# Kernel tuning notes

Hardware: AMD Instinct MI355X
Metric: run time of the kernel (lower is better)

Reference implementation:

```python
import jax, jax.numpy as jnp
import numpy as np

B, C, Himg, Wimg = 32, 256, 64, 64
P = 8            # partition (window) size
HEADS, DH = 8, 32
SEQ = P * P      # tokens per window = 64
SCALE = C ** (-0.5)  # note: feat_dim**-0.5, as in the source
EPS = 1e-5


def _relative_position_index(h, w):
    coords = np.stack(np.meshgrid(np.arange(h), np.arange(w), indexing='ij'))  # [2,h,w]
    cf = coords.reshape(2, -1)
    rel = cf[:, :, None] - cf[:, None, :]            # [2,hw,hw]
    rel = rel.transpose(1, 2, 0)
    rel[:, :, 0] += h - 1
    rel[:, :, 1] += w - 1
    rel[:, :, 0] *= 2 * w - 1
    return rel.sum(-1)                               # [hw,hw] int

REL_IDX = jnp.asarray(_relative_position_index(P, P).reshape(-1))  # [SEQ*SEQ]


def layernorm(x, g, b):
    mu = jnp.mean(x, -1, keepdims=True)
    var = jnp.mean(jnp.square(x - mu), -1, keepdims=True)
    return (x - mu) * jax.lax.rsqrt(var + EPS) * g + b


def setup_inputs() -> dict:
    key = jax.random.key(0)
    ks = jax.random.split(key, 12)
    d = {}
    d['x'] = jax.random.normal(ks[0], (B, C, Himg, Wimg), jnp.float32)
    d['ln1_g'] = jnp.ones((C,), jnp.float32)
    d['ln1_b'] = jnp.zeros((C,), jnp.float32)
    d['qkv_w'] = jax.random.normal(ks[1], (C, 3 * C), jnp.float32) * 0.02
    d['qkv_b'] = jnp.zeros((3 * C,), jnp.float32)
    d['merge_w'] = jax.random.normal(ks[2], (C, C), jnp.float32) * 0.02
    d['merge_b'] = jnp.zeros((C,), jnp.float32)
    d['bias_table'] = jax.random.normal(ks[3], ((2 * P - 1) * (2 * P - 1), HEADS), jnp.float32) * 0.02
    d['ln2_g'] = jnp.ones((C,), jnp.float32)
    d['ln2_b'] = jnp.zeros((C,), jnp.float32)
    d['mlp_w1'] = jax.random.normal(ks[4], (C, 4 * C), jnp.float32) * 0.02
    d['mlp_b1'] = jnp.zeros((4 * C,), jnp.float32)
    d['mlp_w2'] = jax.random.normal(ks[5], (4 * C, C), jnp.float32) * 0.02
    d['mlp_b2'] = jnp.zeros((C,), jnp.float32)
    return d


def reference(x, ln1_g, ln1_b, qkv_w, qkv_b, merge_w, merge_b, bias_table,
              ln2_g, ln2_b, mlp_w1, mlp_b1, mlp_w2, mlp_b2):
    Bn, Cn, H, W = x.shape
    hp, wp = H // P, W // P
    # window partition: [B,C,H,W] -> [B, G, P*P, C]
    xw = x.reshape(Bn, Cn, hp, P, wp, P).transpose(0, 2, 4, 3, 5, 1)
    xw = xw.reshape(Bn, hp * wp, P * P, Cn)

    # --- attention block ---
    h = layernorm(xw, ln1_g, ln1_b)
    qkv = h @ qkv_w + qkv_b                                    # [B,G,S,3C]
    q, k, v = jnp.split(qkv, 3, axis=-1)
    def heads(t):
        return t.reshape(Bn, hp * wp, SEQ, HEADS, DH).transpose(0, 1, 3, 2, 4)
    q, k, v = heads(q), heads(k) * SCALE, heads(v)             # [B,G,h,S,d]
    scores = jnp.einsum('bghid,bghjd->bghij', q, k)            # [B,G,h,S,S]
    rel_bias = bias_table[REL_IDX].reshape(SEQ, SEQ, HEADS).transpose(2, 0, 1)
    attn = jax.nn.softmax(scores + rel_bias[None, None], axis=-1)
    out = jnp.einsum('bghij,bghjd->bghid', attn, v)            # [B,G,h,S,d]
    out = out.transpose(0, 1, 3, 2, 4).reshape(Bn, hp * wp, SEQ, Cn)
    xw = xw + (out @ merge_w + merge_b)

    # --- MLP block ---
    h = layernorm(xw, ln2_g, ln2_b)
    h = jax.nn.gelu(h @ mlp_w1 + mlp_b1, approximate=False)
    xw = xw + (h @ mlp_w2 + mlp_b2)

    # window departition: [B,G,P*P,C] -> [B,C,H,W]
    y = xw.reshape(Bn, hp, wp, P, P, Cn).transpose(0, 5, 1, 3, 2, 4)
    return y.reshape(Bn, Cn, hp * P, wp * P)
```

## Files before the change

kernel.cpp:

```cpp
#include <hip/hip_runtime.h>

typedef __attribute__((ext_vector_type(8))) short short8;
typedef __attribute__((ext_vector_type(8))) unsigned short ushort8v;
typedef __attribute__((ext_vector_type(4))) float f32x4;
typedef __attribute__((ext_vector_type(4))) int int4v;
typedef __attribute__((ext_vector_type(4))) unsigned short ushort4v;
typedef __attribute__((ext_vector_type(2))) unsigned short ushort2v;

#define SCALE_F 0.0625f
#define EPS_F 1e-5f

__device__ __forceinline__ float bf2f(unsigned short u) {
  unsigned int i = ((unsigned int)u) << 16;
  return __builtin_bit_cast(float, i);
}
__device__ __forceinline__ unsigned short f2bf(float f) {
  unsigned int i = __builtin_bit_cast(unsigned int, f);
  i += 0x7fffu + ((i >> 16) & 1u);
  return (unsigned short)(i >> 16);
}

__device__ __forceinline__ void gload_lds16(const unsigned short* g, unsigned short* l) {
  __builtin_amdgcn_global_load_lds(
      (const __attribute__((address_space(1))) void*)g,
      (__attribute__((address_space(3))) void*)l, 16, 0, 0);
}

template<int K, int N>
__global__ void cast_wt(const float* __restrict__ src, unsigned short* __restrict__ dst) {
  int id = blockIdx.x * 256 + threadIdx.x;
  if (id >= K * N) return;
  int k = id % K, n = id / K;
  dst[id] = f2bf(src[(size_t)k * N + n]);
}

__global__ void build_relb(const float* __restrict__ table, float* __restrict__ relb) {
  int id = blockIdx.x * 256 + threadIdx.x;
  int h = id >> 12, i = (id >> 6) & 63, j = id & 63;
  int dy = (i >> 3) - (j >> 3) + 7;
  int dx = (i & 7) - (j & 7) + 7;
  relb[id] = table[(dy * 15 + dx) * 8 + h];
}

#define PLN_RS 264
__global__ __launch_bounds__(256) void part_ln1(
    const float* __restrict__ x, const float* __restrict__ g, const float* __restrict__ bb,
    unsigned short* __restrict__ h) {
  __shared__ __align__(16) unsigned short t_lds[128 * PLN_RS];
  __shared__ float ps_sum[128][2];
  __shared__ float ps_ss[128][2];
  const int tid = threadIdx.x;
  const int bid = blockIdx.x;
  const int b = bid >> 5, wr = (bid >> 2) & 7, cp = bid & 3;
  const int r0 = wr * 8;
  const int c0 = cp * 16;

  const int q = tid & 3, r = (tid >> 2) & 7, cb = tid >> 5;
  const float* xb = x + (size_t)b * 256 * 4096 + (size_t)(r0 + r) * 64 + c0 + q * 4;
#pragma unroll
  for (int it = 0; it < 16; it++) {
    int cpair = it * 8 + cb;
    const float* p0 = xb + (size_t)(2 * cpair) * 4096;
    f32x4 v0 = *(const f32x4*)p0;
    f32x4 v1 = *(const f32x4*)(p0 + 4096);
#pragma unroll
    for (int j = 0; j < 4; j++) {
      int px = r * 16 + q * 4 + j;
      ushort2v u = { f2bf(v0[j]), f2bf(v1[j]) };
      *(ushort2v*)(&t_lds[px * PLN_RS + 2 * cpair]) = u;
    }
  }
  __syncthreads();

  {
    const int p = tid & 127, half = tid >> 7;
    float sum = 0.f, ss = 0.f;
#pragma unroll
    for (int i = 0; i < 16; i++) {
      ushort8v u = *(const ushort8v*)(&t_lds[p * PLN_RS + half * 128 + i * 8]);
#pragma unroll
      for (int e = 0; e < 8; e++) { float f = bf2f(u[e]); sum += f; ss += f * f; }
    }
    ps_sum[p][half] = sum;
    ps_ss[p][half] = ss;
  }
  __syncthreads();

#pragma unroll
  for (int w = 0; w < 16; w++) {
    int id = w * 256 + tid;
    int p = id >> 5, ch = id & 31;
    float mu = (ps_sum[p][0] + ps_sum[p][1]) * (1.f / 256.f);
    float var = (ps_ss[p][0] + ps_ss[p][1]) * (1.f / 256.f) - mu * mu;
    float rs = rsqrtf(var + EPS_F);
    ushort8v u = *(const ushort8v*)(&t_lds[p * PLN_RS + ch * 8]);
    f32x4 g0 = *(const f32x4*)(g + ch * 8);
    f32x4 g1 = *(const f32x4*)(g + ch * 8 + 4);
    f32x4 b0 = *(const f32x4*)(bb + ch * 8);
    f32x4 b1 = *(const f32x4*)(bb + ch * 8 + 4);
    ushort8v o;
#pragma unroll
    for (int e = 0; e < 4; e++) {
      o[e]     = f2bf((bf2f(u[e])     - mu) * rs * g0[e] + b0[e]);
      o[e + 4] = f2bf((bf2f(u[e + 4]) - mu) * rs * g1[e] + b1[e]);
    }
    int rr = p >> 4, col = p & 15;
    size_t m = (size_t)b * 4096 + (size_t)(wr * 8 + cp * 2 + (col >> 3)) * 64 + rr * 8 + (col & 7);
    *(ushort8v*)(h + m * 256 + ch * 8) = o;
  }
}

__global__ __launch_bounds__(256) void ln2k(
    const unsigned short* __restrict__ x2, const float* __restrict__ g, const float* __restrict__ bb,
    unsigned short* __restrict__ h2) {
  int m = blockIdx.x * 4 + (threadIdx.x >> 6);
  int l = threadIdx.x & 63;
  ushort4v u = *(const ushort4v*)(x2 + (size_t)m * 256 + l * 4);
  float v[4];
  float sum = 0.f, ss = 0.f;
#pragma unroll
  for (int j = 0; j < 4; j++) { v[j] = bf2f(u[j]); sum += v[j]; ss += v[j] * v[j]; }
#pragma unroll
  for (int d = 1; d < 64; d <<= 1) {
    sum += __shfl_xor(sum, d, 64);
    ss  += __shfl_xor(ss, d, 64);
  }
  float mu = sum * (1.f / 256.f);
  float var = ss * (1.f / 256.f) - mu * mu;
  float rs = rsqrtf(var + EPS_F);
  ushort4v oh;
#pragma unroll
  for (int j = 0; j < 4; j++) {
    int c = l * 4 + j;
    oh[j] = f2bf((v[j] - mu) * rs * g[c] + bb[c]);
  }
  *(ushort4v*)(h2 + (size_t)m * 256 + l * 4) = oh;
}

enum { EPI_QKV = 0, EPI_MERGE = 1, EPI_GELU = 2, EPI_OUT = 3 };

template<int EPI>
__device__ __forceinline__ void gemm_body(
    unsigned short* As, unsigned short* Bs,
    const unsigned short* __restrict__ A, const unsigned short* __restrict__ Bt,
    const float* __restrict__ bias, const void* __restrict__ res,
    void* __restrict__ out, int K, int N, long m_base) {
  const int tid = threadIdx.x;
  const int l15 = tid & 15, lhi = (tid & 63) >> 4;
  const int wid = tid >> 6, wm = wid >> 1, wn = wid & 1;
  const size_t m0 = (size_t)blockIdx.x * 128;
  const int n0 = blockIdx.y * 128;
  const int row_s = tid >> 3, kc8 = (tid & 7) * 8;

  auto stage = [&](int kb, int k0) {
#pragma unroll
    for (int i = 0; i < 4; i++) {
      int row = i * 32 + row_s;
      gload_lds16(A + (m0 + row) * (size_t)K + k0 + kc8, &As[kb * 8192 + (i * 256 + tid) * 8]);
      gload_lds16(Bt + (size_t)(n0 + row) * (size_t)K + k0 + kc8, &Bs[kb * 8192 + (i * 256 + tid) * 8]);
    }
  };

  f32x4 acc[4][4];
#pragma unroll
  for (int i = 0; i < 4; i++)
#pragma unroll
    for (int j = 0; j < 4; j++) acc[i][j] = (f32x4){0.f, 0.f, 0.f, 0.f};

  stage(0, 0);
  int kb = 0;
  for (int k0 = 0; k0 < K; k0 += 64, kb ^= 1) {
    if (k0 + 64 < K) {
      stage(kb ^ 1, k0 + 64);
      asm volatile("s_waitcnt vmcnt(8)" ::: "memory");
    } else {
      asm volatile("s_waitcnt vmcnt(0)" ::: "memory");
    }
    __builtin_amdgcn_s_barrier();
#pragma unroll
    for (int ks = 0; ks < 2; ks++) {
      short8 af[4], bfr[4];
#pragma unroll
      for (int t = 0; t < 4; t++) {
        af[t]  = *(const short8*)(&As[kb * 8192 + (wm * 64 + t * 16 + l15) * 64 + ks * 32 + lhi * 8]);
        bfr[t] = *(const short8*)(&Bs[kb * 8192 + (wn * 64 + t * 16 + l15) * 64 + ks * 32 + lhi * 8]);
      }
#pragma unroll
      for (int mt = 0; mt < 4; mt++)
#pragma unroll
        for (int nt = 0; nt < 4; nt++)
          acc[mt][nt] = __builtin_amdgcn_mfma_f32_16x16x32_bf16(af[mt], bfr[nt], acc[mt][nt], 0, 0, 0);
    }
    __builtin_amdgcn_s_barrier();
  }

#pragma unroll
  for (int mt = 0; mt < 4; mt++) {
#pragma unroll
    for (int nt = 0; nt < 4; nt++) {
      const size_t gml0 = m0 + wm * 64 + mt * 16 + lhi * 4;
      const size_t gm0 = gml0 + (size_t)m_base;
      const int gn = n0 + wn * 64 + nt * 16 + l15;
      if (EPI == EPI_QKV) {
#pragma unroll
        for (int r = 0; r < 4; r++)
          ((unsigned short*)out)[(gml0 + r) * (size_t)N + gn] = f2bf(acc[mt][nt][r] + bias[gn]);
      } else if (EPI == EPI_MERGE) {
        int bi = (int)(gm0 >> 12), gg = (int)((gm0 >> 6) & 63), s0 = (int)(gm0 & 63);
        size_t sp = (size_t)((gg >> 3) * 8 + (s0 >> 3)) * 64 + (gg & 7) * 8 + (s0 & 7);
        f32x4 xr = *(const f32x4*)(&((const float*)res)[((size_t)(bi * 256 + gn)) * 4096 + sp]);
#pragma unroll
        for (int r = 0; r < 4; r++)
          ((unsigned short*)out)[(gm0 + r) * 256 + gn] = f2bf(acc[mt][nt][r] + bias[gn] + xr[r]);
      } else if (EPI == EPI_GELU) {
#pragma unroll
        for (int r = 0; r < 4; r++) {
          float v = acc[mt][nt][r] + bias[gn];
          float gl = 0.5f * v * (1.f + erff(v * 0.70710678118f));
          ((unsigned short*)out)[(gml0 + r) * (size_t)N + gn] = f2bf(gl);
        }
      } else {
        int bi = (int)(gm0 >> 12), gg = (int)((gm0 >> 6) & 63), s0 = (int)(gm0 & 63);
        size_t sp = (size_t)((gg >> 3) * 8 + (s0 >> 3)) * 64 + (gg & 7) * 8 + (s0 & 7);
        f32x4 o4;
#pragma unroll
        for (int r = 0; r < 4; r++)
          o4[r] = acc[mt][nt][r] + bias[gn] + bf2f(((const unsigned short*)res)[(gm0 + r) * 256 + gn]);
        *(f32x4*)(&((float*)out)[((size_t)(bi * 256 + gn)) * 4096 + sp]) = o4;
      }
    }
  }
}

#define GEMM_WRAP(name, epi)                                                          \
__global__ __launch_bounds__(256) void name(                                          \
    const unsigned short* __restrict__ A, const unsigned short* __restrict__ Bt,      \
    const float* __restrict__ bias, const void* __restrict__ res,                     \
    void* __restrict__ out, int K, int N, long m_base) {                              \
  __shared__ __align__(16) unsigned short As[2 * 128 * 64];                           \
  __shared__ __align__(16) unsigned short Bs[2 * 128 * 64];                           \
  gemm_body<epi>(As, Bs, A, Bt, bias, res, out, K, N, m_base);                        \
}
GEMM_WRAP(gemm_qkv, EPI_QKV)
GEMM_WRAP(gemm_merge, EPI_MERGE)
GEMM_WRAP(gemm_gelu, EPI_GELU)
GEMM_WRAP(gemm_out, EPI_OUT)

__global__ __launch_bounds__(64) void attn_k(
    const unsigned short* __restrict__ qkv, const float* __restrict__ relb,
    unsigned short* __restrict__ o) {
  __shared__ __align__(16) unsigned short p_lds[64 * 72];
  __shared__ __align__(16) unsigned short vt_lds[32 * 72];
  const int l = threadIdx.x;
  const int l15 = l & 15, lhi = l >> 4;
  const int w = blockIdx.x, head = blockIdx.y;
  const unsigned short* base = qkv + (size_t)w * 64 * 768 + head * 32;

  short8 aq[4], bk[4];
#pragma unroll
  for (int t = 0; t < 4; t++) {
    aq[t] = *(const short8*)(base + (t * 16 + l15) * 768 + lhi * 8);
    bk[t] = *(const short8*)(base + 256 + (t * 16 + l15) * 768 + lhi * 8);
  }
  f32x4 s[4][4];
#pragma unroll
  for (int i = 0; i < 4; i++)
#pragma unroll
    for (int j = 0; j < 4; j++) s[i][j] = (f32x4){0.f, 0.f, 0.f, 0.f};
#pragma unroll
  for (int mt = 0; mt < 4; mt++)
#pragma unroll
    for (int nt = 0; nt < 4; nt++)
      s[mt][nt] = __builtin_amdgcn_mfma_f32_16x16x32_bf16(aq[mt], bk[nt], s[mt][nt], 0, 0, 0);

  const float* rb = relb + head * 4096;
  float rsum[4][4];
#pragma unroll
  for (int mt = 0; mt < 4; mt++) {
#pragma unroll
    for (int r = 0; r < 4; r++) {
      int row = mt * 16 + lhi * 4 + r;
      float vv[4];
      float vmax = -1e30f;
#pragma unroll
      for (int nt = 0; nt < 4; nt++) {
        int col = nt * 16 + l15;
        float v = s[mt][nt][r] * SCALE_F + rb[row * 64 + col];
        vv[nt] = v;
        vmax = fmaxf(vmax, v);
      }
#pragma unroll
      for (int d = 1; d < 16; d <<= 1) vmax = fmaxf(vmax, __shfl_xor(vmax, d, 64));
      float sum = 0.f;
#pragma unroll
      for (int nt = 0; nt < 4; nt++) {
        float p = __expf(vv[nt] - vmax);
        sum += p;
        p_lds[row * 72 + nt * 16 + l15] = f2bf(p);
      }
#pragma unroll
      for (int d = 1; d < 16; d <<= 1) sum += __shfl_xor(sum, d, 64);
      rsum[mt][r] = 1.f / sum;
    }
  }

#pragma unroll
  for (int j = 0; j < 4; j++) {
    short8 vv = *(const short8*)(base + 512 + l * 768 + j * 8);
#pragma unroll
    for (int e = 0; e < 8; e++)
      vt_lds[(j * 8 + e) * 72 + l] = (unsigned short)vv[e];
  }
  __syncthreads();

  f32x4 o2[4][2];
#pragma unroll
  for (int i = 0; i < 4; i++) { o2[i][0] = (f32x4){0.f,0.f,0.f,0.f}; o2[i][1] = (f32x4){0.f,0.f,0.f,0.f}; }
#pragma unroll
  for (int ks = 0; ks < 2; ks++) {
    short8 ap[4], bv[2];
#pragma unroll
    for (int t = 0; t < 4; t++)
      ap[t] = *(const short8*)(&p_lds[(t * 16 + l15) * 72 + ks * 32 + lhi * 8]);
#pragma unroll
    for (int t = 0; t < 2; t++)
      bv[t] = *(const short8*)(&vt_lds[(t * 16 + l15) * 72 + ks * 32 + lhi * 8]);
#pragma unroll
    for (int mt = 0; mt < 4; mt++)
#pragma unroll
      for (int n2 = 0; n2 < 2; n2++)
        o2[mt][n2] = __builtin_amdgcn_mfma_f32_16x16x32_bf16(ap[mt], bv[n2], o2[mt][n2], 0, 0, 0);
  }
#pragma unroll
  for (int mt = 0; mt < 4; mt++)
#pragma unroll
    for (int n2 = 0; n2 < 2; n2++)
#pragma unroll
      for (int r = 0; r < 4; r++) {
        int row = mt * 16 + lhi * 4 + r;
        int dh = n2 * 16 + l15;
        o[((size_t)w * 64 + row) * 256 + head * 32 + dh] = f2bf(o2[mt][n2][r] * rsum[mt][r]);
      }
}

extern "C" void kernel_launch(void* const* d_in, const int* in_sizes, int n_in,
                              void* d_out, int out_size, void* d_ws, size_t ws_size,
                              hipStream_t stream) {
  (void)in_sizes; (void)n_in; (void)out_size;
  const float* x          = (const float*)d_in[0];
  const float* ln1_g      = (const float*)d_in[1];
  const float* ln1_b      = (const float*)d_in[2];
  const float* qkv_w      = (const float*)d_in[3];
  const float* qkv_b      = (const float*)d_in[4];
  const float* merge_w    = (const float*)d_in[5];
  const float* merge_b    = (const float*)d_in[6];
  const float* bias_table = (const float*)d_in[7];
  const float* ln2_g      = (const float*)d_in[8];
  const float* ln2_b      = (const float*)d_in[9];
  const float* mlp_w1     = (const float*)d_in[10];
  const float* mlp_b1     = (const float*)d_in[11];
  const float* mlp_w2     = (const float*)d_in[12];
  const float* mlp_b2     = (const float*)d_in[13];

  const size_t MB = 1024ull * 1024ull;
  char* ws = (char*)d_ws;
  unsigned short* buf0 = (unsigned short*)(ws);
  unsigned short* x2   = (unsigned short*)(ws + 64 * MB);
  unsigned short* wqkv = (unsigned short*)(ws + 128 * MB);
  unsigned short* wmrg = wqkv + 768 * 256;
  unsigned short* w1t  = wmrg + 256 * 256;
  unsigned short* w2t  = w1t + 1024 * 256;
  float* relb          = (float*)(w2t + 256 * 1024);
  unsigned short* Cbuf = (unsigned short*)(ws + 130 * MB);

  size_t avail = ws_size > 130 * MB ? ws_size - 130 * MB : 0;
  int wc = 64;
  {
    const int cands[3] = {512, 256, 128};
    for (int i = 0; i < 3; i++)
      if ((size_t)cands[i] * 64 * 768 * 2 <= avail) { wc = cands[i]; break; }
  }
  int rc = 2048;
  {
    const int cands[4] = {32768, 16384, 8192, 4096};
    for (int i = 0; i < 4; i++)
      if ((size_t)cands[i] * 1024 * 2 <= avail) { rc = cands[i]; break; }
  }

  cast_wt<256, 768><<<768, 256, 0, stream>>>(qkv_w, wqkv);
  cast_wt<256, 256><<<256, 256, 0, stream>>>(merge_w, wmrg);
  cast_wt<256, 1024><<<1024, 256, 0, stream>>>(mlp_w1, w1t);
  cast_wt<1024, 256><<<1024, 256, 0, stream>>>(mlp_w2, w2t);
  build_relb<<<128, 256, 0, stream>>>(bias_table, relb);

  part_ln1<<<1024, 256, 0, stream>>>(x, ln1_g, ln1_b, buf0);

  for (int w0 = 0; w0 < 2048; w0 += wc) {
    gemm_qkv<<<dim3(wc * 64 / 128, 6), 256, 0, stream>>>(
        buf0 + (size_t)w0 * 64 * 256, wqkv, qkv_b, nullptr, Cbuf, 256, 768, 0);
    attn_k<<<dim3(wc, 8), 64, 0, stream>>>(Cbuf, relb, buf0 + (size_t)w0 * 64 * 256);
  }

  gemm_merge<<<dim3(1024, 2), 256, 0, stream>>>(
      buf0, wmrg, merge_b, x, x2, 256, 256, 0);

  ln2k<<<32768, 256, 0, stream>>>(x2, ln2_g, ln2_b, buf0);

  for (long r0 = 0; r0 < 131072; r0 += rc) {
    gemm_gelu<<<dim3(rc / 128, 8), 256, 0, stream>>>(
        buf0 + (size_t)r0 * 256, w1t, mlp_b1, nullptr, Cbuf, 256, 1024, 0);
    gemm_out<<<dim3(rc / 128, 2), 256, 0, stream>>>(
        Cbuf, w2t, mlp_b2, x2, d_out, 1024, 256, r0);
  }
}
```

Before: 777.3 us.

## Fuse MLP up-projection, GELU and down-projection into one kernel

Replaces the chunked pair of MLP GEMM launches with a single kernel. Each block owns 64 rows: it stages the LN2 output in swizzled LDS, computes the hidden layer in 128-wide slices with GELU written to LDS, and accumulates the down-projection in registers before the residual add and departition store. This removes the round trip of the 131072x1024 hidden activation through global memory and cuts launch count. In exchange, weight B-fragments are read directly from global memory without LDS staging, and each block covers only 64 rows, which may reduce MFMA efficiency.

```diff
diff --git a/kernel.cpp b/kernel.cpp
--- a/kernel.cpp
+++ b/kernel.cpp
@@ -1,6 +1,7 @@
 #include <hip/hip_runtime.h>
 
 typedef __attribute__((ext_vector_type(8))) short short8;
+typedef __attribute__((ext_vector_type(4))) short short4v;
 typedef __attribute__((ext_vector_type(8))) unsigned short ushort8v;
 typedef __attribute__((ext_vector_type(4))) float f32x4;
 typedef __attribute__((ext_vector_type(4))) int int4v;
@@ -137,7 +138,7 @@
   *(ushort4v*)(h2 + (size_t)m * 256 + l * 4) = oh;
 }
 
-enum { EPI_QKV = 0, EPI_MERGE = 1, EPI_GELU = 2, EPI_OUT = 3 };
+enum { EPI_QKV = 0, EPI_MERGE = 1 };
 
 template<int EPI>
 __device__ __forceinline__ void gemm_body(
@@ -205,28 +206,13 @@
 #pragma unroll
         for (int r = 0; r < 4; r++)
           ((unsigned short*)out)[(gml0 + r) * (size_t)N + gn] = f2bf(acc[mt][nt][r] + bias[gn]);
-      } else if (EPI == EPI_MERGE) {
+      } else {
         int bi = (int)(gm0 >> 12), gg = (int)((gm0 >> 6) & 63), s0 = (int)(gm0 & 63);
         size_t sp = (size_t)((gg >> 3) * 8 + (s0 >> 3)) * 64 + (gg & 7) * 8 + (s0 & 7);
         f32x4 xr = *(const f32x4*)(&((const float*)res)[((size_t)(bi * 256 + gn)) * 4096 + sp]);
 #pragma unroll
         for (int r = 0; r < 4; r++)
           ((unsigned short*)out)[(gm0 + r) * 256 + gn] = f2bf(acc[mt][nt][r] + bias[gn] + xr[r]);
-      } else if (EPI == EPI_GELU) {
-#pragma unroll
-        for (int r = 0; r < 4; r++) {
-          float v = acc[mt][nt][r] + bias[gn];
-          float gl = 0.5f * v * (1.f + erff(v * 0.70710678118f));
-          ((unsigned short*)out)[(gml0 + r) * (size_t)N + gn] = f2bf(gl);
-        }
-      } else {
-        int bi = (int)(gm0 >> 12), gg = (int)((gm0 >> 6) & 63), s0 = (int)(gm0 & 63);
-        size_t sp = (size_t)((gg >> 3) * 8 + (s0 >> 3)) * 64 + (gg & 7) * 8 + (s0 & 7);
-        f32x4 o4;
-#pragma unroll
-        for (int r = 0; r < 4; r++)
-          o4[r] = acc[mt][nt][r] + bias[gn] + bf2f(((const unsigned short*)res)[(gm0 + r) * 256 + gn]);
-        *(f32x4*)(&((float*)out)[((size_t)(bi * 256 + gn)) * 4096 + sp]) = o4;
       }
     }
   }
@@ -243,8 +229,111 @@
 }
 GEMM_WRAP(gemm_qkv, EPI_QKV)
 GEMM_WRAP(gemm_merge, EPI_MERGE)
-GEMM_WRAP(gemm_gelu, EPI_GELU)
-GEMM_WRAP(gemm_out, EPI_OUT)
+
+#define A2S 132
+__global__ __launch_bounds__(256, 2) void mlp_fused(
+    const unsigned short* __restrict__ h2, const unsigned short* __restrict__ w1t,
+    const float* __restrict__ b1, const unsigned short* __restrict__ w2t,
+    const float* __restrict__ b2, const unsigned short* __restrict__ x2,
+    float* __restrict__ out) {
+  __shared__ __align__(16) unsigned short Ash[64 * 256];
+  __shared__ __align__(16) unsigned short A2sh[64 * A2S];
+  const int tid = threadIdx.x;
+  const int wid = tid >> 6, l = tid & 63, l15 = l & 15, lhi = l >> 4;
+  const size_t m0 = (size_t)blockIdx.x * 64;
+
+#pragma unroll
+  for (int i = 0; i < 8; i++) {
+    int uidx = i * 256 + tid;
+    int row = uidx >> 5, su = uidx & 31;
+    int gu = su ^ ((row & 15) << 1);
+    gload_lds16(h2 + (m0 + row) * 256 + gu * 8, &Ash[uidx * 8]);
+  }
+  asm volatile("s_waitcnt vmcnt(0)" ::: "memory");
+  __builtin_amdgcn_s_barrier();
+
+  f32x4 oacc[4][4];
+#pragma unroll
+  for (int i = 0; i < 4; i++)
+#pragma unroll
+    for (int j = 0; j < 4; j++) oacc[i][j] = (f32x4){0.f, 0.f, 0.f, 0.f};
+
+  for (int hs = 0; hs < 8; hs++) {
+    f32x4 hacc[4][2];
+#pragma unroll
+    for (int i = 0; i < 4; i++) { hacc[i][0] = (f32x4){0.f,0.f,0.f,0.f}; hacc[i][1] = (f32x4){0.f,0.f,0.f,0.f}; }
+    const int hc0 = hs * 128 + wid * 32;
+#pragma unroll
+    for (int kst = 0; kst < 8; kst++) {
+      short8 af[4], bf1[2];
+#pragma unroll
+      for (int mt = 0; mt < 4; mt++) {
+        int su = (kst * 4 + lhi) ^ ((l15 & 15) << 1);
+        af[mt] = *(const short8*)(&Ash[(mt * 16 + l15) * 256 + su * 8]);
+      }
+#pragma unroll
+      for (int nt = 0; nt < 2; nt++)
+        bf1[nt] = *(const short8*)(w1t + (size_t)(hc0 + nt * 16 + l15) * 256 + kst * 32 + lhi * 8);
+#pragma unroll
+      for (int mt = 0; mt < 4; mt++)
+#pragma unroll
+        for (int nt = 0; nt < 2; nt++)
+          hacc[mt][nt] = __builtin_amdgcn_mfma_f32_16x16x32_bf16(af[mt], bf1[nt], hacc[mt][nt], 0, 0, 0);
+    }
+    float bv0 = b1[hc0 + l15], bv1 = b1[hc0 + 16 + l15];
+#pragma unroll
+    for (int mt = 0; mt < 4; mt++)
+#pragma unroll
+      for (int nt = 0; nt < 2; nt++) {
+        float bv = nt ? bv1 : bv0;
+        int kh = wid * 32 + nt * 16 + l15;
+#pragma unroll
+        for (int rr = 0; rr < 4; rr++) {
+          float v = hacc[mt][nt][rr] + bv;
+          float gl = 0.5f * v * (1.f + erff(v * 0.70710678118f));
+          A2sh[(mt * 16 + lhi * 4 + rr) * A2S + kh] = f2bf(gl);
+        }
+      }
+    __builtin_amdgcn_s_barrier();
+#pragma unroll
+    for (int k2 = 0; k2 < 4; k2++) {
+      short8 a2[4], bf2v[4];
+#pragma unroll
+      for (int mt = 0; mt < 4; mt++) {
+        const unsigned short* p = &A2sh[(mt * 16 + l15) * A2S + k2 * 32 + lhi * 8];
+        short4v lo = *(const short4v*)p;
+        short4v hi = *(const short4v*)(p + 4);
+        a2[mt] = (short8){lo[0], lo[1], lo[2], lo[3], hi[0], hi[1], hi[2], hi[3]};
+      }
+#pragma unroll
+      for (int nt = 0; nt < 4; nt++)
+        bf2v[nt] = *(const short8*)(w2t + (size_t)(wid * 64 + nt * 16 + l15) * 1024 +
+                                    hs * 128 + k2 * 32 + lhi * 8);
+#pragma unroll
+      for (int mt = 0; mt < 4; mt++)
+#pragma unroll
+        for (int nt = 0; nt < 4; nt++)
+          oacc[mt][nt] = __builtin_amdgcn_mfma_f32_16x16x32_bf16(a2[mt], bf2v[nt], oacc[mt][nt], 0, 0, 0);
+    }
+    __builtin_amdgcn_s_barrier();
+  }
+
+#pragma unroll
+  for (int mt = 0; mt < 4; mt++) {
+#pragma unroll
+    for (int nt = 0; nt < 4; nt++) {
+      size_t gm0 = m0 + mt * 16 + lhi * 4;
+      int gn = wid * 64 + nt * 16 + l15;
+      int bi = (int)(gm0 >> 12), gg = (int)((gm0 >> 6) & 63), s0 = (int)(gm0 & 63);
+      size_t sp = (size_t)((gg >> 3) * 8 + (s0 >> 3)) * 64 + (gg & 7) * 8 + (s0 & 7);
+      f32x4 o4;
+#pragma unroll
+      for (int r = 0; r < 4; r++)
+        o4[r] = oacc[mt][nt][r] + b2[gn] + bf2f(x2[(gm0 + r) * 256 + gn]);
+      *(f32x4*)(&out[((size_t)(bi * 256 + gn)) * 4096 + sp]) = o4;
+    }
+  }
+}
 
 __global__ __launch_bounds__(64) void attn_k(
     const unsigned short* __restrict__ qkv, const float* __restrict__ relb,
@@ -380,12 +469,6 @@
     for (int i = 0; i < 3; i++)
       if ((size_t)cands[i] * 64 * 768 * 2 <= avail) { wc = cands[i]; break; }
   }
-  int rc = 2048;
-  {
-    const int cands[4] = {32768, 16384, 8192, 4096};
-    for (int i = 0; i < 4; i++)
-      if ((size_t)cands[i] * 1024 * 2 <= avail) { rc = cands[i]; break; }
-  }
 
   cast_wt<256, 768><<<768, 256, 0, stream>>>(qkv_w, wqkv);
   cast_wt<256, 256><<<256, 256, 0, stream>>>(merge_w, wmrg);
@@ -406,10 +489,5 @@
 
   ln2k<<<32768, 256, 0, stream>>>(x2, ln2_g, ln2_b, buf0);
 
-  for (long r0 = 0; r0 < 131072; r0 += rc) {
-    gemm_gelu<<<dim3(rc / 128, 8), 256, 0, stream>>>(
-        buf0 + (size_t)r0 * 256, w1t, mlp_b1, nullptr, Cbuf, 256, 1024, 0);
-    gemm_out<<<dim3(rc / 128, 2), 256, 0, stream>>>(
-        Cbuf, w2t, mlp_b2, x2, d_out, 1024, 256, r0);
-  }
-}
+  mlp_fused<<<2048, 256, 0, stream>>>(buf0, w1t, mlp_b1, w2t, mlp_b2, x2, (float*)d_out);
+}
```

Result: faster. 747.2 us (-3.9%).

## Fuse MLP up-projection, GELU and down-projection into one kernel

Applied to the files above, without the earlier changes.

Replaces the chunked gemm_gelu/gemm_out pair with a single kernel in which each wave keeps 16 rows of LN2 output in registers, computes 32-wide hidden slices with MFMA, applies GELU, stages them through a small per-wave LDS buffer and accumulates the down-projection directly. This removes the round trip of the 4C hidden activation through global memory and the per-chunk launches. It also swaps exact erf GELU for a tanh-style exp approximation. Weights are now read straight from global memory with no LDS tiling, and each wave holds 16 output accumulators, so register pressure and L2 weight traffic may rise.

```diff
diff --git a/kernel.cpp b/kernel.cpp
--- a/kernel.cpp
+++ b/kernel.cpp
@@ -1,6 +1,7 @@
 #include <hip/hip_runtime.h>
 
 typedef __attribute__((ext_vector_type(8))) short short8;
+typedef __attribute__((ext_vector_type(4))) short short4v;
 typedef __attribute__((ext_vector_type(8))) unsigned short ushort8v;
 typedef __attribute__((ext_vector_type(4))) float f32x4;
 typedef __attribute__((ext_vector_type(4))) int int4v;
@@ -18,6 +19,14 @@
   unsigned int i = __builtin_bit_cast(unsigned int, f);
   i += 0x7fffu + ((i >> 16) & 1u);
   return (unsigned short)(i >> 16);
+}
+
+__device__ __forceinline__ float fast_gelu(float v) {
+  float s = v * v;
+  float u = v * __builtin_fmaf(s, 0.0713548163f, 1.5957691216f);
+  float e = __expf(u);
+  float r = __builtin_amdgcn_rcpf(e + 1.f);
+  return v - v * r;
 }
 
 __device__ __forceinline__ void gload_lds16(const unsigned short* g, unsigned short* l) {
@@ -137,7 +146,7 @@
   *(ushort4v*)(h2 + (size_t)m * 256 + l * 4) = oh;
 }
 
-enum { EPI_QKV = 0, EPI_MERGE = 1, EPI_GELU = 2, EPI_OUT = 3 };
+enum { EPI_QKV = 0, EPI_MERGE = 1 };
 
 template<int EPI>
 __device__ __forceinline__ void gemm_body(
@@ -205,28 +214,13 @@
 #pragma unroll
         for (int r = 0; r < 4; r++)
           ((unsigned short*)out)[(gml0 + r) * (size_t)N + gn] = f2bf(acc[mt][nt][r] + bias[gn]);
-      } else if (EPI == EPI_MERGE) {
+      } else {
         int bi = (int)(gm0 >> 12), gg = (int)((gm0 >> 6) & 63), s0 = (int)(gm0 & 63);
         size_t sp = (size_t)((gg >> 3) * 8 + (s0 >> 3)) * 64 + (gg & 7) * 8 + (s0 & 7);
         f32x4 xr = *(const f32x4*)(&((const float*)res)[((size_t)(bi * 256 + gn)) * 4096 + sp]);
 #pragma unroll
         for (int r = 0; r < 4; r++)
           ((unsigned short*)out)[(gm0 + r) * 256 + gn] = f2bf(acc[mt][nt][r] + bias[gn] + xr[r]);
-      } else if (EPI == EPI_GELU) {
-#pragma unroll
-        for (int r = 0; r < 4; r++) {
-          float v = acc[mt][nt][r] + bias[gn];
-          float gl = 0.5f * v * (1.f + erff(v * 0.70710678118f));
-          ((unsigned short*)out)[(gml0 + r) * (size_t)N + gn] = f2bf(gl);
-        }
-      } else {
-        int bi = (int)(gm0 >> 12), gg = (int)((gm0 >> 6) & 63), s0 = (int)(gm0 & 63);
-        size_t sp = (size_t)((gg >> 3) * 8 + (s0 >> 3)) * 64 + (gg & 7) * 8 + (s0 & 7);
-        f32x4 o4;
-#pragma unroll
-        for (int r = 0; r < 4; r++)
-          o4[r] = acc[mt][nt][r] + bias[gn] + bf2f(((const unsigned short*)res)[(gm0 + r) * 256 + gn]);
-        *(f32x4*)(&((float*)out)[((size_t)(bi * 256 + gn)) * 4096 + sp]) = o4;
       }
     }
   }
@@ -243,8 +237,77 @@
 }
 GEMM_WRAP(gemm_qkv, EPI_QKV)
 GEMM_WRAP(gemm_merge, EPI_MERGE)
-GEMM_WRAP(gemm_gelu, EPI_GELU)
-GEMM_WRAP(gemm_out, EPI_OUT)
+
+#define MLP_ST 40
+__global__ __launch_bounds__(256) void mlp_fused(
+    const unsigned short* __restrict__ h2, const unsigned short* __restrict__ w1t,
+    const float* __restrict__ b1, const unsigned short* __restrict__ w2t,
+    const float* __restrict__ b2, const unsigned short* __restrict__ x2,
+    float* __restrict__ out) {
+  __shared__ __align__(16) unsigned short a2_lds[4][16 * MLP_ST];
+  const int tid = threadIdx.x;
+  const int wid = tid >> 6, l = tid & 63, l15 = l & 15, lhi = l >> 4;
+  const size_t m0 = (size_t)blockIdx.x * 64 + wid * 16;
+  unsigned short* my_lds = a2_lds[wid];
+
+  short8 af[8];
+#pragma unroll
+  for (int kst = 0; kst < 8; kst++)
+    af[kst] = *(const short8*)(h2 + (m0 + l15) * 256 + kst * 32 + lhi * 8);
+
+  f32x4 oacc[16];
+#pragma unroll
+  for (int i = 0; i < 16; i++) oacc[i] = (f32x4){0.f, 0.f, 0.f, 0.f};
+
+  for (int hs = 0; hs < 32; hs++) {
+    const int hc0 = hs * 32;
+    f32x4 hacc0 = (f32x4){0.f, 0.f, 0.f, 0.f};
+    f32x4 hacc1 = (f32x4){0.f, 0.f, 0.f, 0.f};
+#pragma unroll
+    for (int kst = 0; kst < 8; kst++) {
+      short8 w1f0 = *(const short8*)(w1t + (size_t)(hc0 + l15) * 256 + kst * 32 + lhi * 8);
+      short8 w1f1 = *(const short8*)(w1t + (size_t)(hc0 + 16 + l15) * 256 + kst * 32 + lhi * 8);
+      hacc0 = __builtin_amdgcn_mfma_f32_16x16x32_bf16(w1f0, af[kst], hacc0, 0, 0, 0);
+      hacc1 = __builtin_amdgcn_mfma_f32_16x16x32_bf16(w1f1, af[kst], hacc1, 0, 0, 0);
+    }
+    {
+      f32x4 b1v0 = *(const f32x4*)(b1 + hc0 + lhi * 4);
+      f32x4 b1v1 = *(const f32x4*)(b1 + hc0 + 16 + lhi * 4);
+      ushort4v pk0, pk1;
+#pragma unroll
+      for (int r = 0; r < 4; r++) {
+        pk0[r] = f2bf(fast_gelu(hacc0[r] + b1v0[r]));
+        pk1[r] = f2bf(fast_gelu(hacc1[r] + b1v1[r]));
+      }
+      *(ushort4v*)(&my_lds[l15 * MLP_ST + lhi * 4])      = pk0;
+      *(ushort4v*)(&my_lds[l15 * MLP_ST + 16 + lhi * 4]) = pk1;
+    }
+    short8 a2 = *(const short8*)(&my_lds[l15 * MLP_ST + lhi * 8]);
+#pragma unroll
+    for (int ng = 0; ng < 4; ng++) {
+      short8 w2f[4];
+#pragma unroll
+      for (int j = 0; j < 4; j++)
+        w2f[j] = *(const short8*)(w2t + (size_t)((ng * 4 + j) * 16 + l15) * 1024 + hc0 + lhi * 8);
+#pragma unroll
+      for (int j = 0; j < 4; j++)
+        oacc[ng * 4 + j] = __builtin_amdgcn_mfma_f32_16x16x32_bf16(a2, w2f[j], oacc[ng * 4 + j], 0, 0, 0);
+    }
+  }
+
+#pragma unroll
+  for (int nt = 0; nt < 16; nt++) {
+    size_t gm0 = m0 + lhi * 4;
+    int gn = nt * 16 + l15;
+    int bi = (int)(gm0 >> 12), gg = (int)((gm0 >> 6) & 63), s0 = (int)(gm0 & 63);
+    size_t sp = (size_t)((gg >> 3) * 8 + (s0 >> 3)) * 64 + (gg & 7) * 8 + (s0 & 7);
+    f32x4 o4;
+#pragma unroll
+    for (int r = 0; r < 4; r++)
+      o4[r] = oacc[nt][r] + b2[gn] + bf2f(x2[(gm0 + r) * 256 + gn]);
+    *(f32x4*)(&out[((size_t)(bi * 256 + gn)) * 4096 + sp]) = o4;
+  }
+}
 
 __global__ __launch_bounds__(64) void attn_k(
     const unsigned short* __restrict__ qkv, const float* __restrict__ relb,
@@ -380,12 +443,6 @@
     for (int i = 0; i < 3; i++)
       if ((size_t)cands[i] * 64 * 768 * 2 <= avail) { wc = cands[i]; break; }
   }
-  int rc = 2048;
-  {
-    const int cands[4] = {32768, 16384, 8192, 4096};
-    for (int i = 0; i < 4; i++)
-      if ((size_t)cands[i] * 1024 * 2 <= avail) { rc = cands[i]; break; }
-  }
 
   cast_wt<256, 768><<<768, 256, 0, stream>>>(qkv_w, wqkv);
   cast_wt<256, 256><<<256, 256, 0, stream>>>(merge_w, wmrg);
@@ -406,10 +463,5 @@
 
   ln2k<<<32768, 256, 0, stream>>>(x2, ln2_g, ln2_b, buf0);
 
-  for (long r0 = 0; r0 < 131072; r0 += rc) {
-    gemm_gelu<<<dim3(rc / 128, 8), 256, 0, stream>>>(
-        buf0 + (size_t)r0 * 256, w1t, mlp_b1, nullptr, Cbuf, 256, 1024, 0);
-    gemm_out<<<dim3(rc / 128, 2), 256, 0, stream>>>(
-        Cbuf, w2t, mlp_b2, x2, d_out, 1024, 256, r0);
-  }
-}
+  mlp_fused<<<2048, 256, 0, stream>>>(buf0, w1t, mlp_b1, w2t, mlp_b2, x2, (float*)d_out);
+}
```

Measured after the change: 1.345 ms. +73.1%, slower.
